# Kernel tuning notes

Measured on AMD Instinct MI355X. Metric: run time of the kernel, lower is better.

## Reference

```python
import jax, jax.numpy as jnp
import numpy as np

T, D, E = 8192, 1024, 64
CAPACITY_FACTOR = 2.0
CAP = int(CAPACITY_FACTOR * np.ceil(T / E))  # 256 (training-mode capacity)
EPS = 1e-4


def setup_inputs() -> dict:
    key = jax.random.key(0)
    k1, k2, k3 = jax.random.split(key, 3)
    x = jax.random.normal(k1, (T, D), dtype=jnp.float32)
    W_red = jax.random.normal(k2, (D, 4), dtype=jnp.float32) * 0.02
    centroids = jax.random.normal(k3, (E, 4), dtype=jnp.float32)
    return {"x": x, "W_red": W_red, "centroids": centroids}


def reference(x, W_red, centroids):
    # dim reduction (nn.Linear(model_dim, 4, bias=False))
    red = x @ W_red  # [T, 4]
    # cosine logits: centroids are L2-normalized inside _cosine (the in-place
    # 1.5/norm rescale of the parameter cancels under F.normalize)
    c = centroids.astype(jnp.float32)
    cn = c / jnp.maximum(jnp.linalg.norm(c, axis=1, keepdims=True), EPS)
    logits = red.astype(jnp.float32) @ cn.T  # [T, E]
    # _make_finite
    finite = jnp.isfinite(logits)
    fmin = jnp.min(jnp.where(finite, logits, jnp.inf))
    logits = jnp.where(finite, logits, fmin)

    gates = jax.nn.softmax(logits, axis=1)                 # [T, E]
    idx1 = jnp.argmax(gates, axis=1)                       # [T]
    mask1 = jax.nn.one_hot(idx1, E, dtype=gates.dtype)     # [T, E]
    expert_counts = jnp.sum(mask1, axis=0).astype(jnp.int32)  # metadata

    gates1_s = 1.5 * jnp.sum(gates * mask1, axis=1)        # [T]
    loc1 = jnp.cumsum(mask1, axis=0) - 1.0                 # positions within expert

    me = jnp.mean(gates, axis=0)
    ce = jnp.mean(mask1, axis=0)
    l_aux = jnp.mean(me * ce) * (E * E)

    mask1 = mask1 * (loc1 < CAP).astype(mask1.dtype)       # drop overflow tokens
    loc1_s = jnp.sum(loc1 * mask1, axis=1).astype(jnp.int32)  # [T]
    gates1 = gates1_s[:, None] * mask1                     # [T, E]
    loc_sc = jax.nn.one_hot(loc1_s, CAP, dtype=gates1.dtype)  # [T, CAP]
    combine = gates1[:, :, None] * loc_sc[:, None, :]      # [T, E, CAP]
    dispatch_mask = combine != 0
    return (l_aux, combine.astype(x.dtype), dispatch_mask, expert_counts)
```

## Files before the change

kernel.cpp:

```cpp
#include <hip/hip_runtime.h>

#define T 8192
#define D 1024
#define E 64
#define CAP 256

typedef float f32x4 __attribute__((ext_vector_type(4)));

#define TEC ((size_t)134217728)
#define C_OFF   ((size_t)1)
#define M_OFF   ((size_t)1 + TEC)
#define CNT_OFF ((size_t)1 + 2 * TEC)

__global__ __launch_bounds__(256) void k1_gate(
    const float* __restrict__ x, const float* __restrict__ Wred,
    const float* __restrict__ cent, int* __restrict__ idx1,
    float* __restrict__ g15, float* __restrict__ Sg, int* __restrict__ bc)
{
    __shared__ float wcol[4 * D];
    __shared__ float cn[E * 4];
    __shared__ float sg[E];
    const int tid = threadIdx.x;

    for (int i = tid; i < 4 * D; i += 256) {
        int d = i >> 2, c = i & 3;
        wcol[c * D + d] = Wred[i];
    }
    if (tid < E) {
        float c0 = cent[tid * 4 + 0];
        float c1 = cent[tid * 4 + 1];
        float c2 = cent[tid * 4 + 2];
        float c3 = cent[tid * 4 + 3];
        float n = fmaxf(sqrtf(c0 * c0 + c1 * c1 + c2 * c2 + c3 * c3), 1e-4f);
        cn[tid * 4 + 0] = c0 / n;
        cn[tid * 4 + 1] = c1 / n;
        cn[tid * 4 + 2] = c2 / n;
        cn[tid * 4 + 3] = c3 / n;
        sg[tid] = 0.0f;
    }
    __syncthreads();

    const f32x4* __restrict__ wc4 = (const f32x4*)wcol;
    const int wave = tid >> 6, lane = tid & 63;
    for (int it = 0; it < 4; ++it) {
        const int t = blockIdx.x * 16 + it * 4 + wave;
        const f32x4* __restrict__ xr4 = (const f32x4*)(x + (size_t)t * D);
        float a0 = 0.f, a1 = 0.f, a2 = 0.f, a3 = 0.f;
        #pragma unroll
        for (int k = 0; k < 4; ++k) {
            const int i = k * 64 + lane;
            const f32x4 xv = xr4[i];
            const f32x4 w0 = wc4[0 * 256 + i];
            const f32x4 w1 = wc4[1 * 256 + i];
            const f32x4 w2 = wc4[2 * 256 + i];
            const f32x4 w3 = wc4[3 * 256 + i];
            a0 += xv[0] * w0[0] + xv[1] * w0[1] + xv[2] * w0[2] + xv[3] * w0[3];
            a1 += xv[0] * w1[0] + xv[1] * w1[1] + xv[2] * w1[2] + xv[3] * w1[3];
            a2 += xv[0] * w2[0] + xv[1] * w2[1] + xv[2] * w2[2] + xv[3] * w2[3];
            a3 += xv[0] * w3[0] + xv[1] * w3[1] + xv[2] * w3[2] + xv[3] * w3[3];
        }
        #pragma unroll
        for (int off = 32; off; off >>= 1) {
            a0 += __shfl_xor(a0, off);
            a1 += __shfl_xor(a1, off);
            a2 += __shfl_xor(a2, off);
            a3 += __shfl_xor(a3, off);
        }
        float logit = a0 * cn[lane * 4 + 0] + a1 * cn[lane * 4 + 1]
                    + a2 * cn[lane * 4 + 2] + a3 * cn[lane * 4 + 3];
        float m = logit;
        #pragma unroll
        for (int off = 32; off; off >>= 1) m = fmaxf(m, __shfl_xor(m, off));
        unsigned long long ball = __ballot(logit == m);
        int amax = __ffsll(ball) - 1;
        float ev = expf(logit - m);
        float s = ev;
        #pragma unroll
        for (int off = 32; off; off >>= 1) s += __shfl_xor(s, off);
        atomicAdd(&sg[lane], ev / s);
        if (lane == 0) {
            idx1[t] = amax;
            g15[t] = 1.5f / s;
            atomicAdd(&bc[(t >> 8) * E + amax], 1);
        }
    }
    __syncthreads();
    if (tid < E) atomicAdd(&Sg[tid], sg[tid]);
}

__global__ __launch_bounds__(256) void k5_prefix_patch(
    const int* __restrict__ idx1, const float* __restrict__ g15,
    const int* __restrict__ bc, const float* __restrict__ Sg,
    float* __restrict__ out)
{
    __shared__ int pfe[E];
    __shared__ int cwf[256];
    const int tid = threadIdx.x;
    const int chunk = blockIdx.x;
    const int t = chunk * 256 + tid;
    const int e = idx1[t];

    if (tid < E) {
        int run = 0;
        for (int b = 0; b < chunk; ++b) run += bc[b * E + tid];
        pfe[tid] = run;
    }
    cwf[tid] = 0;
    __syncthreads();

    const int wave = tid >> 6, lane = tid & 63;
    unsigned long long same = ~0ull;
    #pragma unroll
    for (int b = 0; b < 6; ++b) {
        unsigned long long bal = __ballot(((e >> b) & 1) != 0);
        same &= ((e >> b) & 1) ? bal : ~bal;
    }
    const unsigned long long below = ((unsigned long long)1 << lane) - 1ull;
    const int rank_in_wave = __popcll(same & below);
    if ((same & below) == 0ull) cwf[wave * E + e] = __popcll(same);
    __syncthreads();

    int rank = pfe[e] + rank_in_wave;
    if (wave > 0) rank += cwf[0 * E + e];
    if (wave > 1) rank += cwf[1 * E + e];
    if (wave > 2) rank += cwf[2 * E + e];

    if (rank < CAP) {
        const size_t row = (size_t)t * (E * CAP) + (size_t)e * CAP + rank;
        out[C_OFF + row] = g15[t];
        out[M_OFF + row] = 1.0f;
    }

    if (chunk == 31 && tid < E) {
        int total = pfe[tid] + bc[31 * E + tid];
        out[CNT_OFF + tid] = (float)total;
        float v = Sg[tid] * (float)total;
        #pragma unroll
        for (int off = 32; off; off >>= 1) v += __shfl_xor(v, off);
        if (tid == 0) out[0] = v * ((float)E / ((float)T * (float)T));
    }
}

extern "C" void kernel_launch(void* const* d_in, const int* in_sizes, int n_in,
                              void* d_out, int out_size, void* d_ws, size_t ws_size,
                              hipStream_t stream)
{
    const float* x    = (const float*)d_in[0];
    const float* Wred = (const float*)d_in[1];
    const float* cent = (const float*)d_in[2];
    float* out = (float*)d_out;

    char* ws = (char*)d_ws;
    int*   idx1 = (int*)ws;
    float* g15  = (float*)(ws + 32768);
    float* Sg   = (float*)(ws + 65536);
    int*   bc   = (int*)(ws + 65536 + 256);

    (void)hipMemsetAsync(d_out, 0, (size_t)out_size, stream);
    (void)hipMemsetAsync(Sg, 0, 256 + 32 * E * sizeof(int), stream);

    k1_gate<<<512, 256, 0, stream>>>(x, Wred, cent, idx1, g15, Sg, bc);
    k5_prefix_patch<<<32, 256, 0, stream>>>(idx1, g15, bc, Sg, out);
}
```

Before: 932.8 us.

## Fuse gating and prefix-scatter kernels into one cooperative kernel with grid syncs

Merges the gate kernel and the prefix/scatter kernel into a single cooperative launch that uses grid-wide syncs. Per-block histograms and gate sums are now written to workspace without global atomics, then reduced hierarchically, which also removes the small memset of the accumulators. This drops one kernel launch and one memset, but adds two grid barriers. The run time is dominated by the large memset of the output (about 1 GB), so the achievable saving is small.

New measurement: 1.072 ms. +15.0%, slower.

```diff
diff --git a/kernel.cpp b/kernel.cpp
--- a/kernel.cpp
+++ b/kernel.cpp
@@ -1,4 +1,7 @@
 #include <hip/hip_runtime.h>
+#include <hip/hip_cooperative_groups.h>
+
+namespace cg = cooperative_groups;
 
 #define T 8192
 #define D 1024
@@ -12,15 +15,18 @@
 #define M_OFF   ((size_t)1 + TEC)
 #define CNT_OFF ((size_t)1 + 2 * TEC)
 
-__global__ __launch_bounds__(256) void k1_gate(
+__global__ __launch_bounds__(256) void kfused(
     const float* __restrict__ x, const float* __restrict__ Wred,
     const float* __restrict__ cent, int* __restrict__ idx1,
-    float* __restrict__ g15, float* __restrict__ Sg, int* __restrict__ bc)
+    float* __restrict__ g15, int* __restrict__ bcb, float* __restrict__ sgb,
+    int* __restrict__ bc32, float* __restrict__ sgc, float* __restrict__ out)
 {
     __shared__ float wcol[4 * D];
     __shared__ float cn[E * 4];
     __shared__ float sg[E];
+    __shared__ int   hh[E];
     const int tid = threadIdx.x;
+    const int bid = blockIdx.x;
 
     for (int i = tid; i < 4 * D; i += 256) {
         int d = i >> 2, c = i & 3;
@@ -37,13 +43,14 @@
         cn[tid * 4 + 2] = c2 / n;
         cn[tid * 4 + 3] = c3 / n;
         sg[tid] = 0.0f;
+        hh[tid] = 0;
     }
     __syncthreads();
 
     const f32x4* __restrict__ wc4 = (const f32x4*)wcol;
     const int wave = tid >> 6, lane = tid & 63;
     for (int it = 0; it < 4; ++it) {
-        const int t = blockIdx.x * 16 + it * 4 + wave;
+        const int t = bid * 16 + it * 4 + wave;
         const f32x4* __restrict__ xr4 = (const f32x4*)(x + (size_t)t * D);
         float a0 = 0.f, a1 = 0.f, a2 = 0.f, a3 = 0.f;
         #pragma unroll
@@ -81,63 +88,80 @@
         if (lane == 0) {
             idx1[t] = amax;
             g15[t] = 1.5f / s;
-            atomicAdd(&bc[(t >> 8) * E + amax], 1);
+            atomicAdd(&hh[amax], 1);
         }
     }
     __syncthreads();
-    if (tid < E) atomicAdd(&Sg[tid], sg[tid]);
-}
-
-__global__ __launch_bounds__(256) void k5_prefix_patch(
-    const int* __restrict__ idx1, const float* __restrict__ g15,
-    const int* __restrict__ bc, const float* __restrict__ Sg,
-    float* __restrict__ out)
-{
-    __shared__ int pfe[E];
-    __shared__ int cwf[256];
-    const int tid = threadIdx.x;
-    const int chunk = blockIdx.x;
-    const int t = chunk * 256 + tid;
-    const int e = idx1[t];
-
     if (tid < E) {
-        int run = 0;
-        for (int b = 0; b < chunk; ++b) run += bc[b * E + tid];
-        pfe[tid] = run;
-    }
-    cwf[tid] = 0;
-    __syncthreads();
-
-    const int wave = tid >> 6, lane = tid & 63;
-    unsigned long long same = ~0ull;
-    #pragma unroll
-    for (int b = 0; b < 6; ++b) {
-        unsigned long long bal = __ballot(((e >> b) & 1) != 0);
-        same &= ((e >> b) & 1) ? bal : ~bal;
-    }
-    const unsigned long long below = ((unsigned long long)1 << lane) - 1ull;
-    const int rank_in_wave = __popcll(same & below);
-    if ((same & below) == 0ull) cwf[wave * E + e] = __popcll(same);
-    __syncthreads();
-
-    int rank = pfe[e] + rank_in_wave;
-    if (wave > 0) rank += cwf[0 * E + e];
-    if (wave > 1) rank += cwf[1 * E + e];
-    if (wave > 2) rank += cwf[2 * E + e];
-
-    if (rank < CAP) {
-        const size_t row = (size_t)t * (E * CAP) + (size_t)e * CAP + rank;
-        out[C_OFF + row] = g15[t];
-        out[M_OFF + row] = 1.0f;
+        bcb[bid * E + tid] = hh[tid];
+        sgb[bid * E + tid] = sg[tid];
     }
 
-    if (chunk == 31 && tid < E) {
-        int total = pfe[tid] + bc[31 * E + tid];
-        out[CNT_OFF + tid] = (float)total;
-        float v = Sg[tid] * (float)total;
+    __threadfence();
+    cg::this_grid().sync();
+
+    if (bid < 32 && tid < E) {
+        int   s1 = 0;
+        float s2 = 0.f;
         #pragma unroll
-        for (int off = 32; off; off >>= 1) v += __shfl_xor(v, off);
-        if (tid == 0) out[0] = v * ((float)E / ((float)T * (float)T));
+        for (int j = 0; j < 16; ++j) {
+            s1 += bcb[(bid * 16 + j) * E + tid];
+            s2 += sgb[(bid * 16 + j) * E + tid];
+        }
+        bc32[bid * E + tid] = s1;
+        sgc [bid * E + tid] = s2;
+    }
+    __threadfence();
+    cg::this_grid().sync();
+
+    if (bid < 32) {
+        __shared__ int pfe[E];
+        __shared__ int cwf[256];
+        const int chunk = bid;
+        const int t2 = chunk * 256 + tid;
+        const int e = idx1[t2];
+
+        if (tid < E) {
+            int run = 0;
+            for (int b = 0; b < chunk; ++b) run += bc32[b * E + tid];
+            pfe[tid] = run;
+        }
+        cwf[tid] = 0;
+        __syncthreads();
+
+        unsigned long long same = ~0ull;
+        #pragma unroll
+        for (int b = 0; b < 6; ++b) {
+            unsigned long long bal = __ballot(((e >> b) & 1) != 0);
+            same &= ((e >> b) & 1) ? bal : ~bal;
+        }
+        const unsigned long long below = ((unsigned long long)1 << lane) - 1ull;
+        const int rank_in_wave = __popcll(same & below);
+        if ((same & below) == 0ull) cwf[wave * E + e] = __popcll(same);
+        __syncthreads();
+
+        int rank = pfe[e] + rank_in_wave;
+        if (wave > 0) rank += cwf[0 * E + e];
+        if (wave > 1) rank += cwf[1 * E + e];
+        if (wave > 2) rank += cwf[2 * E + e];
+
+        if (rank < CAP) {
+            const size_t row = (size_t)t2 * (E * CAP) + (size_t)e * CAP + rank;
+            out[C_OFF + row] = g15[t2];
+            out[M_OFF + row] = 1.0f;
+        }
+
+        if (chunk == 31 && tid < E) {
+            int total = pfe[tid] + bc32[31 * E + tid];
+            out[CNT_OFF + tid] = (float)total;
+            float S = 0.f;
+            #pragma unroll
+            for (int c2 = 0; c2 < 32; ++c2) S += sgc[c2 * E + tid];
+            float v = S * (float)total;
+            #pragma unroll
+            for (int off = 32; off; off >>= 1) v += __shfl_xor(v, off);
+            if (tid == 0) out[0] = v * ((float)E / ((float)T * (float)T));
+        }
     }
 }
 
@@ -153,12 +177,16 @@
     char* ws = (char*)d_ws;
     int*   idx1 = (int*)ws;
     float* g15  = (float*)(ws + 32768);
-    float* Sg   = (float*)(ws + 65536);
-    int*   bc   = (int*)(ws + 65536 + 256);
+    int*   bcb  = (int*)(ws + 65536);
+    float* sgb  = (float*)(ws + 65536 + 131072);
+    int*   bc32 = (int*)(ws + 65536 + 262144);
+    float* sgc  = (float*)(ws + 65536 + 262144 + 8192);
 
     (void)hipMemsetAsync(d_out, 0, (size_t)out_size, stream);
-    (void)hipMemsetAsync(Sg, 0, 256 + 32 * E * sizeof(int), stream);
 
-    k1_gate<<<512, 256, 0, stream>>>(x, Wred, cent, idx1, g15, Sg, bc);
-    k5_prefix_patch<<<32, 256, 0, stream>>>(idx1, g15, bc, Sg, out);
+    void* args[] = {(void*)&x, (void*)&Wred, (void*)&cent, (void*)&idx1,
+                    (void*)&g15, (void*)&bcb, (void*)&sgb, (void*)&bc32,
+                    (void*)&sgc, (void*)&out};
+    (void)hipLaunchCooperativeKernel((void*)kfused, dim3(512), dim3(256),
+                                     args, 0, stream);
 }
```
